# Kernel optimization log

Hardware: AMD Instinct MI355X
Metric: run time of the kernel (lower is better)

The kernel has to match this reference:

```python
import jax, jax.numpy as jnp
import numpy as np

B, S, D, H, T_OUT = 256, 256, 64, 1024, 32  # batch, enc seq, input dim, hidden, decode steps


def setup_inputs() -> dict:
    key = jax.random.key(0)
    ks = jax.random.split(key, 15)
    p = lambda k, shape: jax.random.normal(k, shape, jnp.float32) * 0.05
    return {
        "X": jax.random.normal(ks[0], (B, S, D), jnp.float32),
        # encoder LSTM (2 layers); bias = b_ih + b_hh fused (same math)
        "enc_Wih0": p(ks[1], (4 * H, D)), "enc_Whh0": p(ks[2], (4 * H, H)), "enc_b0": p(ks[3], (4 * H,)),
        "enc_Wih1": p(ks[4], (4 * H, H)), "enc_Whh1": p(ks[5], (4 * H, H)), "enc_b1": p(ks[6], (4 * H,)),
        # decoder LSTM (2 layers, scalar input)
        "dec_Wih0": p(ks[7], (4 * H, 1)), "dec_Whh0": p(ks[8], (4 * H, H)), "dec_b0": p(ks[9], (4 * H,)),
        "dec_Wih1": p(ks[10], (4 * H, H)), "dec_Whh1": p(ks[11], (4 * H, H)), "dec_b1": p(ks[12], (4 * H,)),
        # output projection hidden -> 1
        "fc_W": p(ks[13], (1, H)), "fc_b": p(ks[14], (1,)),
    }


def _cell(x, h, c, Wih, Whh, b):
    # torch LSTM cell, gate order i, f, g, o
    gates = x @ Wih.T + h @ Whh.T + b  # [B, 4H]
    i, f, g, o = jnp.split(gates, 4, axis=-1)
    c = jax.nn.sigmoid(f) * c + jax.nn.sigmoid(i) * jnp.tanh(g)
    h = jax.nn.sigmoid(o) * jnp.tanh(c)
    return h, c


def reference(X, enc_Wih0, enc_Whh0, enc_b0, enc_Wih1, enc_Whh1, enc_b1,
              dec_Wih0, dec_Whh0, dec_b0, dec_Wih1, dec_Whh1, dec_b1,
              fc_W, fc_b):
    batch = X.shape[0]
    zeros = jnp.zeros((batch, H), X.dtype)

    def enc_layer(Wih, Whh, b, xs):  # xs: [S, B, Din]
        def step(carry, x_t):
            h, c = carry
            h, c = _cell(x_t, h, c, Wih, Whh, b)
            return (h, c), h
        (h, c), hs = jax.lax.scan(step, (zeros, zeros), xs)
        return hs, h, c

    xs = jnp.swapaxes(X, 0, 1)  # time-major [S, B, D]
    hs0, h0, c0 = enc_layer(enc_Wih0, enc_Whh0, enc_b0, xs)
    _, h1, c1 = enc_layer(enc_Wih1, enc_Whh1, enc_b1, hs0)

    inp0 = jnp.zeros((batch, 1), X.dtype)

    def dec_step(carry, _):
        dh0, dc0, dh1, dc1, inp = carry
        dh0, dc0 = _cell(inp, dh0, dc0, dec_Wih0, dec_Whh0, dec_b0)
        dh1, dc1 = _cell(dh0, dh1, dc1, dec_Wih1, dec_Whh1, dec_b1)
        pred = dh1 @ fc_W.T + fc_b  # [B, 1]; dropout is identity at inference
        return (dh0, dc0, dh1, dc1, pred), pred

    _, preds = jax.lax.scan(dec_step, (h0, c0, h1, c1, inp0), None, length=T_OUT)
    return jnp.transpose(preds, (1, 0, 2))  # [B, T_OUT, 1]
```

## Files before the change

### kernel.cpp

```cpp
#include <hip/hip_runtime.h>

#define B_ 256
#define S_ 256
#define D_ 64
#define H_ 1024
#define G4 4096
#define TOUT 32

typedef unsigned short u16;
typedef __attribute__((ext_vector_type(8))) short short8;
typedef __attribute__((ext_vector_type(4))) float float4v;

__device__ __forceinline__ float bf2f(u16 b) {
  return __uint_as_float(((unsigned int)b) << 16);
}
__device__ __forceinline__ u16 f2bf(float f) {
  unsigned int u = __float_as_uint(f);
  unsigned int r = (u + 0x7fffu + ((u >> 16) & 1u)) >> 16;
  return (u16)r;
}
__device__ __forceinline__ unsigned pack2(float a, float b) {
  return (unsigned)f2bf(a) | ((unsigned)f2bf(b) << 16);
}
__device__ __forceinline__ float sigm(float x) {
  return 1.f / (1.f + __expf(-x));
}
__device__ __forceinline__ float tanh_(float x) {
  float xc = fminf(fmaxf(x, -15.f), 15.f);
  float e = __expf(2.f * xc);
  return (e - 1.f) / (e + 1.f);
}

__global__ __launch_bounds__(256) void cvt_kernel(const float* __restrict__ src,
                                                  u16* __restrict__ dst, int n) {
  for (int i = blockIdx.x * blockDim.x + threadIdx.x; i < n;
       i += gridDim.x * blockDim.x)
    dst[i] = f2bf(src[i]);
}

__global__ __launch_bounds__(256) void zero_kernel(uint4* __restrict__ p, int n16) {
  for (int i = blockIdx.x * blockDim.x + threadIdx.x; i < n16;
       i += gridDim.x * blockDim.x)
    p[i] = make_uint4(0u, 0u, 0u, 0u);
}

struct LayerDesc {
  const u16* A0; int lda0;
  const u16* A1; int lda1; int klen0;
  const void* W0; int ldw0;
  const void* W1; int ldw1; int Ktot;
  const float* bias;
  const float* wcol;
  const float* inp;
  float* c;
  u16* h;
  int active;
};

template <bool WF32>
__global__ __launch_bounds__(256) void lstm_step_kernel(LayerDesc dA, LayerDesc dB)
{
  const bool second = (blockIdx.y >= 4);
  const LayerDesc d = second ? dB : dA;
  if (!d.active) return;

  __shared__ u16 As[64][72];
  __shared__ u16 Bs[64][72];
  __shared__ float Gs[64][68];

  const int tid = threadIdx.x;
  const int m0 = (second ? (blockIdx.y - 4) : blockIdx.y) * 64;
  const int n0 = blockIdx.x * 64;
  const int ub = n0 >> 2;
  const int r = tid >> 2;
  const int q = tid & 3;
  const int lane = tid & 63;
  const int wv = tid >> 6;
  const int wm = (wv >> 1) * 32;
  const int wn = (wv & 1) * 32;
  const int l16 = lane & 15;
  const int quad = lane >> 4;

  const int klen0 = d.klen0;
  const u16* aw0 = d.A0 + (size_t)(m0 + r) * d.lda0;
  const u16* aw1 = d.A1 + (size_t)(m0 + r) * d.lda1;
  const int orow = (r & 3) * H_ + ub + (r >> 2);
  const u16* bw0_h = (const u16*)d.W0 + (size_t)orow * d.ldw0;
  const u16* bw1_h = (const u16*)d.W1 + (size_t)orow * d.ldw1;
  const float* bw0_f = (const float*)d.W0 + (size_t)orow * d.ldw0;
  const float* bw1_f = (const float*)d.W1 + (size_t)orow * d.ldw1;

  uint4 av0, av1, bv0, bv1;
  float4 bf0, bf1, bf2, bf3;

  auto load_chunk = [&](int kc) {
    const int kg = kc * 64 + q * 16;
    const bool first = kg < klen0;
    const u16* pa = first ? (aw0 + kg) : (aw1 + (kg - klen0));
    av0 = *(const uint4*)pa;
    av1 = *(const uint4*)(pa + 8);
    if constexpr (WF32) {
      const float* pb = first ? (bw0_f + kg) : (bw1_f + (kg - klen0));
      bf0 = *(const float4*)pb;
      bf1 = *(const float4*)(pb + 4);
      bf2 = *(const float4*)(pb + 8);
      bf3 = *(const float4*)(pb + 12);
    } else {
      const u16* pb = first ? (bw0_h + kg) : (bw1_h + (kg - klen0));
      bv0 = *(const uint4*)pb;
      bv1 = *(const uint4*)(pb + 8);
    }
  };

  float4v acc00 = {}, acc01 = {}, acc10 = {}, acc11 = {};
  const int nch = d.Ktot >> 6;
  load_chunk(0);
  for (int kc = 0; kc < nch; ++kc) {
    if constexpr (WF32) {
      bv0 = make_uint4(pack2(bf0.x, bf0.y), pack2(bf0.z, bf0.w),
                       pack2(bf1.x, bf1.y), pack2(bf1.z, bf1.w));
      bv1 = make_uint4(pack2(bf2.x, bf2.y), pack2(bf2.z, bf2.w),
                       pack2(bf3.x, bf3.y), pack2(bf3.z, bf3.w));
    }
    __syncthreads();
    *(uint4*)&As[r][q * 16]     = av0;
    *(uint4*)&As[r][q * 16 + 8] = av1;
    *(uint4*)&Bs[r][q * 16]     = bv0;
    *(uint4*)&Bs[r][q * 16 + 8] = bv1;
    __syncthreads();
    if (kc + 1 < nch) load_chunk(kc + 1);
#pragma unroll
    for (int ks = 0; ks < 2; ++ks) {
      const int kb = ks * 32 + quad * 8;
      short8 a0 = *(const short8*)&As[wm + l16][kb];
      short8 a1 = *(const short8*)&As[wm + 16 + l16][kb];
      short8 b0 = *(const short8*)&Bs[wn + l16][kb];
      short8 b1 = *(const short8*)&Bs[wn + 16 + l16][kb];
      acc00 = __builtin_amdgcn_mfma_f32_16x16x32_bf16(a0, b0, acc00, 0, 0, 0);
      acc01 = __builtin_amdgcn_mfma_f32_16x16x32_bf16(a0, b1, acc01, 0, 0, 0);
      acc10 = __builtin_amdgcn_mfma_f32_16x16x32_bf16(a1, b0, acc10, 0, 0, 0);
      acc11 = __builtin_amdgcn_mfma_f32_16x16x32_bf16(a1, b1, acc11, 0, 0, 0);
    }
  }

#pragma unroll
  for (int rr = 0; rr < 4; ++rr) {
    Gs[wm + quad * 4 + rr][wn + l16]           = acc00[rr];
    Gs[wm + quad * 4 + rr][wn + 16 + l16]      = acc01[rr];
    Gs[wm + 16 + quad * 4 + rr][wn + l16]      = acc10[rr];
    Gs[wm + 16 + quad * 4 + rr][wn + 16 + l16] = acc11[rr];
  }
  __syncthreads();

#pragma unroll
  for (int it = 0; it < 4; ++it) {
    const int p = tid + it * 256;
    const int bl = p >> 4;
    const int u = p & 15;
    const int J = ub + u;
    const int bg = m0 + bl;
    const float4v g = *(const float4v*)&Gs[bl][u * 4];
    float pi = g[0] + d.bias[J];
    float pf = g[1] + d.bias[H_ + J];
    float pg = g[2] + d.bias[2 * H_ + J];
    float po = g[3] + d.bias[3 * H_ + J];
    if (d.inp != nullptr) {
      const float iv = d.inp[bg];
      pi += iv * d.wcol[J];
      pf += iv * d.wcol[H_ + J];
      pg += iv * d.wcol[2 * H_ + J];
      po += iv * d.wcol[3 * H_ + J];
    }
    const size_t idx = (size_t)bg * H_ + J;
    const float c = d.c[idx];
    const float cn = sigm(pf) * c + sigm(pi) * tanh_(pg);
    d.c[idx] = cn;
    d.h[idx] = f2bf(sigm(po) * tanh_(cn));
  }
}

__global__ __launch_bounds__(256) void fc_kernel(
    const u16* __restrict__ h1, const float* __restrict__ fcW,
    const float* __restrict__ fcb, float* __restrict__ out,
    float* __restrict__ inp, int t)
{
  const int b = blockIdx.x;
  const int tid = threadIdx.x;
  const u16* hr = h1 + (size_t)b * H_ + tid * 4;
  const float* wr = fcW + tid * 4;
  float s = 0.f;
#pragma unroll
  for (int j = 0; j < 4; ++j) s += bf2f(hr[j]) * wr[j];
#pragma unroll
  for (int off = 32; off > 0; off >>= 1) s += __shfl_down(s, off, 64);
  __shared__ float red[4];
  if ((tid & 63) == 0) red[tid >> 6] = s;
  __syncthreads();
  if (tid == 0) {
    const float p = red[0] + red[1] + red[2] + red[3] + fcb[0];
    out[(size_t)b * TOUT + t] = p;
    inp[b] = p;
  }
}

extern "C" void kernel_launch(void* const* d_in, const int* in_sizes, int n_in,
                              void* d_out, int out_size, void* d_ws, size_t ws_size,
                              hipStream_t stream)
{
  const float* X     = (const float*)d_in[0];
  const float* eWih0 = (const float*)d_in[1];
  const float* eWhh0 = (const float*)d_in[2];
  const float* eb0   = (const float*)d_in[3];
  const float* eWih1 = (const float*)d_in[4];
  const float* eWhh1 = (const float*)d_in[5];
  const float* eb1   = (const float*)d_in[6];
  const float* dWih0 = (const float*)d_in[7];
  const float* dWhh0 = (const float*)d_in[8];
  const float* db0   = (const float*)d_in[9];
  const float* dWih1 = (const float*)d_in[10];
  const float* dWhh1 = (const float*)d_in[11];
  const float* db1   = (const float*)d_in[12];
  const float* fcW   = (const float*)d_in[13];
  const float* fcb   = (const float*)d_in[14];
  float* out = (float*)d_out;

  char* ws = (char*)d_ws;
  size_t off = 0;
  auto alloc = [&](size_t bytes) -> void* {
    void* p = ws + off;
    off += (bytes + 255) & ~(size_t)255;
    return p;
  };
  u16* h0buf[2], *h1buf[2];
  h0buf[0] = (u16*)alloc((size_t)B_ * H_ * 2);
  h0buf[1] = (u16*)alloc((size_t)B_ * H_ * 2);
  h1buf[0] = (u16*)alloc((size_t)B_ * H_ * 2);
  h1buf[1] = (u16*)alloc((size_t)B_ * H_ * 2);
  float* C0  = (float*)alloc((size_t)B_ * H_ * 4);
  float* C1  = (float*)alloc((size_t)B_ * H_ * 4);
  float* INP = (float*)alloc(B_ * 4);
  const size_t zbytes = off;
  u16* XB = (u16*)alloc((size_t)B_ * S_ * D_ * 2);
  u16* WB_eWih0 = (u16*)alloc((size_t)G4 * D_ * 2);
  u16* WB_eWhh0 = (u16*)alloc((size_t)G4 * H_ * 2);
  u16* WB_eWih1 = (u16*)alloc((size_t)G4 * H_ * 2);
  u16* WB_eWhh1 = (u16*)alloc((size_t)G4 * H_ * 2);
  u16* WB_dWhh0 = (u16*)alloc((size_t)G4 * H_ * 2);
  u16* WB_dWih1 = (u16*)alloc((size_t)G4 * H_ * 2);
  u16* WB_dWhh1 = (u16*)alloc((size_t)G4 * H_ * 2);
  const size_t need_full = off;
  const bool fast = (ws_size >= need_full);

  zero_kernel<<<dim3(256), dim3(256), 0, stream>>>((uint4*)ws, (int)(zbytes / 16));
  cvt_kernel<<<dim3(1024), dim3(256), 0, stream>>>(X, XB, B_ * S_ * D_);
  if (fast) {
    cvt_kernel<<<dim3(256), dim3(256), 0, stream>>>(eWih0, WB_eWih0, G4 * D_);
    cvt_kernel<<<dim3(1024), dim3(256), 0, stream>>>(eWhh0, WB_eWhh0, G4 * H_);
    cvt_kernel<<<dim3(1024), dim3(256), 0, stream>>>(eWih1, WB_eWih1, G4 * H_);
    cvt_kernel<<<dim3(1024), dim3(256), 0, stream>>>(eWhh1, WB_eWhh1, G4 * H_);
    cvt_kernel<<<dim3(1024), dim3(256), 0, stream>>>(dWhh0, WB_dWhh0, G4 * H_);
    cvt_kernel<<<dim3(1024), dim3(256), 0, stream>>>(dWih1, WB_dWih1, G4 * H_);
    cvt_kernel<<<dim3(1024), dim3(256), 0, stream>>>(dWhh1, WB_dWhh1, G4 * H_);
  }

  auto mk = [&](const u16* A0, int lda0, const u16* A1, int lda1, int klen0,
                const void* W0b, const void* W0f, int ldw0,
                const void* W1b, const void* W1f, int ldw1, int Ktot,
                const float* bias, const float* wcol, const float* inp,
                float* c, u16* h) {
    LayerDesc d;
    d.A0 = A0; d.lda0 = lda0; d.A1 = A1; d.lda1 = lda1; d.klen0 = klen0;
    d.W0 = fast ? W0b : W0f; d.ldw0 = ldw0;
    d.W1 = fast ? W1b : W1f; d.ldw1 = ldw1; d.Ktot = Ktot;
    d.bias = bias; d.wcol = wcol; d.inp = inp; d.c = c; d.h = h;
    d.active = 1;
    return d;
  };
  LayerDesc off_d = {};
  off_d.active = 0;

  auto launch = [&](dim3 grid, const LayerDesc& a, const LayerDesc& b) {
    if (fast)
      lstm_step_kernel<false><<<grid, dim3(256), 0, stream>>>(a, b);
    else
      lstm_step_kernel<true><<<grid, dim3(256), 0, stream>>>(a, b);
  };

  for (int u = 0; u <= S_; ++u) {
    LayerDesc d0 = off_d, d1 = off_d;
    if (u < S_) {
      const int t = u;
      d0 = mk(XB + t * D_, S_ * D_, h0buf[t & 1], H_, D_,
              WB_eWih0, eWih0, D_, WB_eWhh0, eWhh0, H_, 1088,
              eb0, nullptr, nullptr, C0, h0buf[(t + 1) & 1]);
    }
    if (u >= 1) {
      const int t = u - 1;
      d1 = mk(h0buf[(t + 1) & 1], H_, h1buf[t & 1], H_, H_,
              WB_eWih1, eWih1, H_, WB_eWhh1, eWhh1, H_, 2048,
              eb1, nullptr, nullptr, C1, h1buf[(t + 1) & 1]);
    }
    launch(dim3(64, 8), d0, d1);
  }

  for (int t = 0; t < TOUT; ++t) {
    u16* h0i = h0buf[t & 1]; u16* h0o = h0buf[(t + 1) & 1];
    u16* h1i = h1buf[t & 1]; u16* h1o = h1buf[(t + 1) & 1];
    LayerDesc dl0 = mk(h0i, H_, h0i, H_, 1024,
                       WB_dWhh0, dWhh0, H_, WB_dWhh0, dWhh0, H_, 1024,
                       db0, dWih0, INP, C0, h0o);
    launch(dim3(64, 4), dl0, off_d);
    LayerDesc dl1 = mk(h0o, H_, h1i, H_, H_,
                       WB_dWih1, dWih1, H_, WB_dWhh1, dWhh1, H_, 2048,
                       db1, nullptr, nullptr, C1, h1o);
    launch(dim3(64, 4), dl1, off_d);
    fc_kernel<<<dim3(B_), dim3(256), 0, stream>>>(h1o, fcW, fcb, out, INP, t);
  }
}
```

Baseline: 7.263 ms.

## Double-buffer LDS tiles and prefetch two chunks ahead in LSTM step GEMM

Splits the shared-memory A/B tiles into two buffers and keeps two register sets of prefetched global data, so each k-chunk writes the next tile into the alternate buffer while MFMAs consume the current one. This removes one of the two __syncthreads per chunk and gives global loads more time in flight. The cost is extra LDS (two tile buffers), more registers for the second prefetch set, and possibly lower occupancy.

Measured after the change: 8.854 ms. 21.9% more time.

```diff
diff --git a/kernel.cpp b/kernel.cpp
--- a/kernel.cpp
+++ b/kernel.cpp
@@ -64,8 +64,8 @@
   const LayerDesc d = second ? dB : dA;
   if (!d.active) return;
 
-  __shared__ u16 As[64][72];
-  __shared__ u16 Bs[64][72];
+  __shared__ u16 As[2][64][72];
+  __shared__ u16 Bs[2][64][72];
   __shared__ float Gs[64][68];
 
   const int tid = threadIdx.x;
@@ -90,57 +90,77 @@
   const float* bw0_f = (const float*)d.W0 + (size_t)orow * d.ldw0;
   const float* bw1_f = (const float*)d.W1 + (size_t)orow * d.ldw1;
 
-  uint4 av0, av1, bv0, bv1;
-  float4 bf0, bf1, bf2, bf3;
-
-  auto load_chunk = [&](int kc) {
+  uint4 pa0, pa1, pb0, pb1;
+  uint4 qa0, qa1, qb0, qb1;
+  float4 pf0, pf1, pf2, pf3, qf0, qf1, qf2, qf3;
+
+  auto load_to = [&](int kc, uint4& A0r, uint4& A1r, uint4& B0r, uint4& B1r,
+                     float4& F0, float4& F1, float4& F2, float4& F3) {
     const int kg = kc * 64 + q * 16;
     const bool first = kg < klen0;
     const u16* pa = first ? (aw0 + kg) : (aw1 + (kg - klen0));
-    av0 = *(const uint4*)pa;
-    av1 = *(const uint4*)(pa + 8);
+    A0r = *(const uint4*)pa;
+    A1r = *(const uint4*)(pa + 8);
     if constexpr (WF32) {
       const float* pb = first ? (bw0_f + kg) : (bw1_f + (kg - klen0));
-      bf0 = *(const float4*)pb;
-      bf1 = *(const float4*)(pb + 4);
-      bf2 = *(const float4*)(pb + 8);
-      bf3 = *(const float4*)(pb + 12);
+      F0 = *(const float4*)pb;
+      F1 = *(const float4*)(pb + 4);
+      F2 = *(const float4*)(pb + 8);
+      F3 = *(const float4*)(pb + 12);
     } else {
       const u16* pb = first ? (bw0_h + kg) : (bw1_h + (kg - klen0));
-      bv0 = *(const uint4*)pb;
-      bv1 = *(const uint4*)(pb + 8);
-    }
+      B0r = *(const uint4*)pb;
+      B1r = *(const uint4*)(pb + 8);
+    }
+  };
+
+  auto write_to = [&](int buf, uint4& A0r, uint4& A1r, uint4& B0r, uint4& B1r,
+                      float4& F0, float4& F1, float4& F2, float4& F3) {
+    uint4 w0 = B0r, w1 = B1r;
+    if constexpr (WF32) {
+      w0 = make_uint4(pack2(F0.x, F0.y), pack2(F0.z, F0.w),
+                      pack2(F1.x, F1.y), pack2(F1.z, F1.w));
+      w1 = make_uint4(pack2(F2.x, F2.y), pack2(F2.z, F2.w),
+                      pack2(F3.x, F3.y), pack2(F3.z, F3.w));
+    }
+    *(uint4*)&As[buf][r][q * 16]     = A0r;
+    *(uint4*)&As[buf][r][q * 16 + 8] = A1r;
+    *(uint4*)&Bs[buf][r][q * 16]     = w0;
+    *(uint4*)&Bs[buf][r][q * 16 + 8] = w1;
   };
 
   float4v acc00 = {}, acc01 = {}, acc10 = {}, acc11 = {};
-  const int nch = d.Ktot >> 6;
-  load_chunk(0);
-  for (int kc = 0; kc < nch; ++kc) {
-    if constexpr (WF32) {
-      bv0 = make_uint4(pack2(bf0.x, bf0.y), pack2(bf0.z, bf0.w),
-                       pack2(bf1.x, bf1.y), pack2(bf1.z, bf1.w));
-      bv1 = make_uint4(pack2(bf2.x, bf2.y), pack2(bf2.z, bf2.w),
-                       pack2(bf3.x, bf3.y), pack2(bf3.z, bf3.w));
-    }
-    __syncthreads();
-    *(uint4*)&As[r][q * 16]     = av0;
-    *(uint4*)&As[r][q * 16 + 8] = av1;
-    *(uint4*)&Bs[r][q * 16]     = bv0;
-    *(uint4*)&Bs[r][q * 16 + 8] = bv1;
-    __syncthreads();
-    if (kc + 1 < nch) load_chunk(kc + 1);
+  auto mfma_step = [&](int buf) {
 #pragma unroll
     for (int ks = 0; ks < 2; ++ks) {
       const int kb = ks * 32 + quad * 8;
-      short8 a0 = *(const short8*)&As[wm + l16][kb];
-      short8 a1 = *(const short8*)&As[wm + 16 + l16][kb];
-      short8 b0 = *(const short8*)&Bs[wn + l16][kb];
-      short8 b1 = *(const short8*)&Bs[wn + 16 + l16][kb];
+      short8 a0 = *(const short8*)&As[buf][wm + l16][kb];
+      short8 a1 = *(const short8*)&As[buf][wm + 16 + l16][kb];
+      short8 b0 = *(const short8*)&Bs[buf][wn + l16][kb];
+      short8 b1 = *(const short8*)&Bs[buf][wn + 16 + l16][kb];
       acc00 = __builtin_amdgcn_mfma_f32_16x16x32_bf16(a0, b0, acc00, 0, 0, 0);
       acc01 = __builtin_amdgcn_mfma_f32_16x16x32_bf16(a0, b1, acc01, 0, 0, 0);
       acc10 = __builtin_amdgcn_mfma_f32_16x16x32_bf16(a1, b0, acc10, 0, 0, 0);
       acc11 = __builtin_amdgcn_mfma_f32_16x16x32_bf16(a1, b1, acc11, 0, 0, 0);
     }
+  };
+
+  const int nch = d.Ktot >> 6;
+  load_to(0, pa0, pa1, pb0, pb1, pf0, pf1, pf2, pf3);
+  if (nch > 1) load_to(1, qa0, qa1, qb0, qb1, qf0, qf1, qf2, qf3);
+  write_to(0, pa0, pa1, pb0, pb1, pf0, pf1, pf2, pf3);
+  __syncthreads();
+  for (int kc = 0; kc < nch; ++kc) {
+    if ((kc & 1) == 0) {
+      if (kc + 1 < nch) write_to(1, qa0, qa1, qb0, qb1, qf0, qf1, qf2, qf3);
+      if (kc + 2 < nch) load_to(kc + 2, pa0, pa1, pb0, pb1, pf0, pf1, pf2, pf3);
+      mfma_step(0);
+    } else {
+      if (kc + 1 < nch) write_to(0, pa0, pa1, pb0, pb1, pf0, pf1, pf2, pf3);
+      if (kc + 2 < nch) load_to(kc + 2, qa0, qa1, qb0, qb1, qf0, qf1, qf2, qf3);
+      mfma_step(1);
+    }
+    __syncthreads();
   }
 
 #pragma unroll
```

## Split K across waves with direct-to-register MFMA fragment loads and LDS reduction

Applied to the files above, without the earlier changes.

The per-step LSTM GEMM no longer stages A and B tiles through shared memory with per-chunk barriers. Each of the four waves now computes the whole 64x64 output tile over a strided quarter of K, loading MFMA fragments straight from global memory into registers with double buffering. The partial sums are then reduced through shared memory before the gate nonlinearity. This removes the LDS round-trips and syncs in the K loop. In exchange it uses far more accumulator registers (16 float4 per wave), relies on the launch-bounds hint for two blocks per CU, and issues many narrow 16-byte global loads with reduced coalescing.

Measured after the change: 8.600 ms. +18.4%, slower.

```diff
diff --git a/kernel.cpp b/kernel.cpp
--- a/kernel.cpp
+++ b/kernel.cpp
@@ -58,97 +58,115 @@
 };
 
 template <bool WF32>
-__global__ __launch_bounds__(256) void lstm_step_kernel(LayerDesc dA, LayerDesc dB)
+__global__ __launch_bounds__(256, 2) void lstm_step_kernel(LayerDesc dA, LayerDesc dB)
 {
   const bool second = (blockIdx.y >= 4);
   const LayerDesc d = second ? dB : dA;
   if (!d.active) return;
 
-  __shared__ u16 As[64][72];
-  __shared__ u16 Bs[64][72];
-  __shared__ float Gs[64][68];
+  __shared__ float Gs[2][64][64];
 
   const int tid = threadIdx.x;
   const int m0 = (second ? (blockIdx.y - 4) : blockIdx.y) * 64;
   const int n0 = blockIdx.x * 64;
   const int ub = n0 >> 2;
-  const int r = tid >> 2;
-  const int q = tid & 3;
   const int lane = tid & 63;
   const int wv = tid >> 6;
-  const int wm = (wv >> 1) * 32;
-  const int wn = (wv & 1) * 32;
   const int l16 = lane & 15;
   const int quad = lane >> 4;
 
+  const u16* aP0[4]; const u16* aP1[4];
+  const void* bP0[4]; const void* bP1[4];
+#pragma unroll
+  for (int i = 0; i < 4; ++i) {
+    const int am = m0 + i * 16 + l16;
+    aP0[i] = d.A0 + (size_t)am * d.lda0 + quad * 8;
+    aP1[i] = d.A1 + (size_t)am * d.lda1 + quad * 8;
+  }
+#pragma unroll
+  for (int j = 0; j < 4; ++j) {
+    const int p = n0 + j * 16 + l16;
+    const int orow = (p & 3) * H_ + (p >> 2);
+    if constexpr (WF32) {
+      bP0[j] = (const void*)((const float*)d.W0 + (size_t)orow * d.ldw0 + quad * 8);
+      bP1[j] = (const void*)((const float*)d.W1 + (size_t)orow * d.ldw1 + quad * 8);
+    } else {
+      bP0[j] = (const void*)((const u16*)d.W0 + (size_t)orow * d.ldw0 + quad * 8);
+      bP1[j] = (const void*)((const u16*)d.W1 + (size_t)orow * d.ldw1 + quad * 8);
+    }
+  }
+
   const int klen0 = d.klen0;
-  const u16* aw0 = d.A0 + (size_t)(m0 + r) * d.lda0;
-  const u16* aw1 = d.A1 + (size_t)(m0 + r) * d.lda1;
-  const int orow = (r & 3) * H_ + ub + (r >> 2);
-  const u16* bw0_h = (const u16*)d.W0 + (size_t)orow * d.ldw0;
-  const u16* bw1_h = (const u16*)d.W1 + (size_t)orow * d.ldw1;
-  const float* bw0_f = (const float*)d.W0 + (size_t)orow * d.ldw0;
-  const float* bw1_f = (const float*)d.W1 + (size_t)orow * d.ldw1;
-
-  uint4 av0, av1, bv0, bv1;
-  float4 bf0, bf1, bf2, bf3;
-
-  auto load_chunk = [&](int kc) {
-    const int kg = kc * 64 + q * 16;
-    const bool first = kg < klen0;
-    const u16* pa = first ? (aw0 + kg) : (aw1 + (kg - klen0));
-    av0 = *(const uint4*)pa;
-    av1 = *(const uint4*)(pa + 8);
-    if constexpr (WF32) {
-      const float* pb = first ? (bw0_f + kg) : (bw1_f + (kg - klen0));
-      bf0 = *(const float4*)pb;
-      bf1 = *(const float4*)(pb + 4);
-      bf2 = *(const float4*)(pb + 8);
-      bf3 = *(const float4*)(pb + 12);
-    } else {
-      const u16* pb = first ? (bw0_h + kg) : (bw1_h + (kg - klen0));
-      bv0 = *(const uint4*)pb;
-      bv1 = *(const uint4*)(pb + 8);
-    }
-  };
-
-  float4v acc00 = {}, acc01 = {}, acc10 = {}, acc11 = {};
-  const int nch = d.Ktot >> 6;
-  load_chunk(0);
-  for (int kc = 0; kc < nch; ++kc) {
-    if constexpr (WF32) {
-      bv0 = make_uint4(pack2(bf0.x, bf0.y), pack2(bf0.z, bf0.w),
-                       pack2(bf1.x, bf1.y), pack2(bf1.z, bf1.w));
-      bv1 = make_uint4(pack2(bf2.x, bf2.y), pack2(bf2.z, bf2.w),
-                       pack2(bf3.x, bf3.y), pack2(bf3.z, bf3.w));
-    }
-    __syncthreads();
-    *(uint4*)&As[r][q * 16]     = av0;
-    *(uint4*)&As[r][q * 16 + 8] = av1;
-    *(uint4*)&Bs[r][q * 16]     = bv0;
-    *(uint4*)&Bs[r][q * 16 + 8] = bv1;
-    __syncthreads();
-    if (kc + 1 < nch) load_chunk(kc + 1);
-#pragma unroll
-    for (int ks = 0; ks < 2; ++ks) {
-      const int kb = ks * 32 + quad * 8;
-      short8 a0 = *(const short8*)&As[wm + l16][kb];
-      short8 a1 = *(const short8*)&As[wm + 16 + l16][kb];
-      short8 b0 = *(const short8*)&Bs[wn + l16][kb];
-      short8 b1 = *(const short8*)&Bs[wn + 16 + l16][kb];
-      acc00 = __builtin_amdgcn_mfma_f32_16x16x32_bf16(a0, b0, acc00, 0, 0, 0);
-      acc01 = __builtin_amdgcn_mfma_f32_16x16x32_bf16(a0, b1, acc01, 0, 0, 0);
-      acc10 = __builtin_amdgcn_mfma_f32_16x16x32_bf16(a1, b0, acc10, 0, 0, 0);
-      acc11 = __builtin_amdgcn_mfma_f32_16x16x32_bf16(a1, b1, acc11, 0, 0, 0);
-    }
-  }
-
-#pragma unroll
-  for (int rr = 0; rr < 4; ++rr) {
-    Gs[wm + quad * 4 + rr][wn + l16]           = acc00[rr];
-    Gs[wm + quad * 4 + rr][wn + 16 + l16]      = acc01[rr];
-    Gs[wm + 16 + quad * 4 + rr][wn + l16]      = acc10[rr];
-    Gs[wm + 16 + quad * 4 + rr][wn + 16 + l16] = acc11[rr];
+  auto ldfr = [&](int c, short8* fa, short8* fb) {
+    const int k0 = c * 32;
+    const bool f = k0 < klen0;
+    const int ka = f ? k0 : (k0 - klen0);
+#pragma unroll
+    for (int i = 0; i < 4; ++i)
+      fa[i] = *(const short8*)((f ? aP0[i] : aP1[i]) + ka);
+#pragma unroll
+    for (int j = 0; j < 4; ++j) {
+      if constexpr (WF32) {
+        const float* pb = (const float*)(f ? bP0[j] : bP1[j]) + ka;
+        const float4 x0 = *(const float4*)pb;
+        const float4 x1 = *(const float4*)(pb + 4);
+        union { uint4 u; short8 s; } cv;
+        cv.u = make_uint4(pack2(x0.x, x0.y), pack2(x0.z, x0.w),
+                          pack2(x1.x, x1.y), pack2(x1.z, x1.w));
+        fb[j] = cv.s;
+      } else {
+        fb[j] = *(const short8*)((const u16*)(f ? bP0[j] : bP1[j]) + ka);
+      }
+    }
+  };
+
+  float4v acc[4][4];
+#pragma unroll
+  for (int i = 0; i < 4; ++i)
+#pragma unroll
+    for (int j = 0; j < 4; ++j) acc[i][j] = (float4v){0.f, 0.f, 0.f, 0.f};
+
+  auto domfma = [&](short8* fa, short8* fb) {
+#pragma unroll
+    for (int i = 0; i < 4; ++i)
+#pragma unroll
+      for (int j = 0; j < 4; ++j)
+        acc[i][j] = __builtin_amdgcn_mfma_f32_16x16x32_bf16(fa[i], fb[j],
+                                                            acc[i][j], 0, 0, 0);
+  };
+
+  const int nch = d.Ktot >> 5;
+  int c = wv;
+  short8 sa0[4], sb0[4], sa1[4], sb1[4];
+  if (c < nch) ldfr(c, sa0, sb0);
+  while (c < nch) {
+    if (c + 4 < nch) ldfr(c + 4, sa1, sb1);
+    domfma(sa0, sb0);
+    c += 4;
+    if (c >= nch) break;
+    if (c + 4 < nch) ldfr(c + 4, sa0, sb0);
+    domfma(sa1, sb1);
+    c += 4;
+  }
+
+  if (wv < 2) {
+#pragma unroll
+    for (int i = 0; i < 4; ++i)
+#pragma unroll
+      for (int j = 0; j < 4; ++j)
+#pragma unroll
+        for (int rr = 0; rr < 4; ++rr)
+          Gs[wv][i * 16 + quad * 4 + rr][j * 16 + l16] = acc[i][j][rr];
+  }
+  __syncthreads();
+  if (wv >= 2) {
+#pragma unroll
+    for (int i = 0; i < 4; ++i)
+#pragma unroll
+      for (int j = 0; j < 4; ++j)
+#pragma unroll
+        for (int rr = 0; rr < 4; ++rr)
+          Gs[wv - 2][i * 16 + quad * 4 + rr][j * 16 + l16] += acc[i][j][rr];
   }
   __syncthreads();
 
@@ -159,7 +177,8 @@
     const int u = p & 15;
     const int J = ub + u;
     const int bg = m0 + bl;
-    const float4v g = *(const float4v*)&Gs[bl][u * 4];
+    const float4v g = *(const float4v*)&Gs[0][bl][u * 4] +
+                      *(const float4v*)&Gs[1][bl][u * 4];
     float pi = g[0] + d.bias[J];
     float pf = g[1] + d.bias[H_ + J];
     float pg = g[2] + d.bias[2 * H_ + J];
@@ -172,8 +191,8 @@
       po += iv * d.wcol[3 * H_ + J];
     }
     const size_t idx = (size_t)bg * H_ + J;
-    const float c = d.c[idx];
-    const float cn = sigm(pf) * c + sigm(pi) * tanh_(pg);
+    const float cc = d.c[idx];
+    const float cn = sigm(pf) * cc + sigm(pi) * tanh_(pg);
     d.c[idx] = cn;
     d.h[idx] = f2bf(sigm(po) * tanh_(cn));
   }
```
